# Kernel tuning notes

Hardware: AMD Instinct MI355X
Metric: run time of the kernel (lower is better)

Reference implementation:

```python
import jax, jax.numpy as jnp
import numpy as np

N, K, D = 500_000, 256, 64  # points, prototypes, feature dim


def setup_inputs() -> dict:
    key = jax.random.key(0)
    kx, km = jax.random.split(key)
    X = jax.random.normal(kx, (N, D), dtype=jnp.float32)
    mus = jax.random.normal(km, (K, D), dtype=jnp.float32)
    return {"X": X, "mus": mus}


def reference(X, mus):
    # Faithful to vmap(lambda x: argmin(sum((mus - x)**2, axis=1)))(X),
    # but expressed with the Gram-matrix distance trick so the K*D broadcast
    # is a single GEMM instead of an O(N,K,D) elementwise intermediate.
    x_sq = jnp.sum(X * X, axis=1, keepdims=True)        # [N, 1]
    mu_sq = jnp.sum(mus * mus, axis=1)                  # [K]
    d2 = x_sq - 2.0 * (X @ mus.T) + mu_sq[None, :]      # [N, K] squared dists
    return jnp.argmin(d2, axis=1)                       # [N] int assignments
```

## Files before the change

kernel.cpp:

```cpp
#include <hip/hip_runtime.h>


#define DIM 64
#define NPROTO 256
#define NBLK 1024
#define SUBT 4
#define PPI 64
#define MARGIN_ACC 0.005f

using f32x4  = __attribute__((ext_vector_type(4))) float;
using bf16x8 = __attribute__((ext_vector_type(8))) __bf16;
using bf16x4 = __attribute__((ext_vector_type(4))) __bf16;

__device__ __forceinline__ void split2(float x, __bf16& h0, __bf16& h1) {
    h0 = (__bf16)x;
    h1 = (__bf16)(x - (float)h0);
}

__device__ __forceinline__ void stage_one(__bf16* lvl0, float4 v, int wgi) {
    bf16x4 w0, w1;
    const float xf[4] = {v.x, v.y, v.z, v.w};
#pragma unroll
    for (int e = 0; e < 4; ++e) {
        __bf16 h0, h1;
        split2(xf[e], h0, h1);
        w0[e] = h0; w1[e] = h1;
    }
    ((bf16x4*)lvl0)[wgi] = w0;
    ((bf16x4*)(lvl0 + 16 * 64))[wgi] = w1;
}

__device__ __forceinline__ float4 loadx(const float* __restrict__ X, int t,
                                        int j, int srow, int spart, int n) {
    int pr = t * PPI + j * 16 + srow;
    pr = (pr < n) ? pr : (n - 1);
    return *(const float4*)(X + (size_t)pr * DIM + spart * 4);
}

__attribute__((amdgpu_waves_per_eu(3, 4)))
__global__ void __launch_bounds__(256)
argmin_mfma_kernel(const float* __restrict__ X,
                   const float* __restrict__ mus,
                   int* __restrict__ out,
                   unsigned* __restrict__ ws_count,
                   int* __restrict__ ws_list,
                   int use_list, int n) {
    __shared__ __align__(16) __bf16 s_x[2][SUBT][2][16][64];
    __shared__ float s_musq[NPROTO];
    __shared__ float s_cb[2][SUBT][4][16];
    __shared__ float s_cb2[2][SUBT][4][16];
    __shared__ int   s_ck[2][SUBT][4][16];

    const int tid = threadIdx.x;
    const int w  = tid >> 6;
    const int l  = tid & 63;
    const int lp = l & 15;
    const int lg = l >> 4;

    {
        const float4* m4 = (const float4*)(mus + tid * DIM);
        float a0 = 0.f, a1 = 0.f, a2 = 0.f, a3 = 0.f;
#pragma unroll
        for (int q = 0; q < 16; ++q) {
            float4 v = m4[q];
            a0 = fmaf(v.x, v.x, a0); a1 = fmaf(v.y, v.y, a1);
            a2 = fmaf(v.z, v.z, a2); a3 = fmaf(v.w, v.w, a3);
        }
        s_musq[tid] = -0.5f * ((a0 + a1) + (a2 + a3));
    }

    bf16x8 amu[4][2][2];
#pragma unroll
    for (int t = 0; t < 4; ++t) {
        const int p = w * 64 + t * 16 + lp;
#pragma unroll
        for (int h = 0; h < 2; ++h) {
            const float* src = mus + (size_t)p * DIM + h * 32 + lg * 8;
            const float4 va = *(const float4*)src;
            const float4 vb = *(const float4*)(src + 4);
            const float xs[8] = {va.x, va.y, va.z, va.w, vb.x, vb.y, vb.z, vb.w};
            bf16x8 m0, m1;
#pragma unroll
            for (int e = 0; e < 8; ++e) {
                __bf16 h0, h1;
                split2(xs[e], h0, h1);
                m0[e] = h0; m1[e] = h1;
            }
            amu[t][h][0] = m0; amu[t][h][1] = m1;
        }
    }

    const int ntiles = (n + PPI - 1) / PPI;
    const int q = ntiles / NBLK, rr = ntiles % NBLK;
    const int bid = blockIdx.x;
    const int t0  = bid * q + (bid < rr ? bid : rr);
    const int cnt = q + (bid < rr ? 1 : 0);

    const int srow = tid >> 4, spart = tid & 15;
    const int wgi = spart ^ ((srow & 7) << 1);

    float4 xn0 = loadx(X, t0, 0, srow, spart, n);
    float4 xn1 = loadx(X, t0, 1, srow, spart, n);
    float4 xn2 = loadx(X, t0, 2, srow, spart, n);
    float4 xn3 = loadx(X, t0, 3, srow, spart, n);
    stage_one(&s_x[0][0][0][srow][0], xn0, wgi);
    stage_one(&s_x[0][1][0][srow][0], xn1, wgi);
    stage_one(&s_x[0][2][0][srow][0], xn2, wgi);
    stage_one(&s_x[0][3][0][srow][0], xn3, wgi);
    __syncthreads();

    const int kbase = w * 64 + lg * 4;
    f32x4 mh[4];
#pragma unroll
    for (int t = 0; t < 4; ++t)
#pragma unroll
        for (int r = 0; r < 4; ++r)
            mh[t][r] = s_musq[kbase + t * 16 + r];

    for (int it = 0; it < cnt; ++it) {
        const int tile = t0 + it;
        const int par = it & 1;
        const bool more = (it + 1 < cnt);

        if (more) {
            xn0 = loadx(X, tile + 1, 0, srow, spart, n);
            xn1 = loadx(X, tile + 1, 1, srow, spart, n);
            xn2 = loadx(X, tile + 1, 2, srow, spart, n);
            xn3 = loadx(X, tile + 1, 3, srow, spart, n);
        }

#pragma unroll
        for (int j = 0; j < SUBT; ++j) {
            bf16x8 bx[2][2];
#pragma unroll
            for (int h = 0; h < 2; ++h)
#pragma unroll
                for (int v = 0; v < 2; ++v)
                    bx[h][v] = ((const bf16x8*)&s_x[par][j][v][lp][0])
                                   [(h * 4 + lg) ^ (lp & 7)];

            f32x4 acc[4];
#pragma unroll
            for (int t = 0; t < 4; ++t)
                acc[t] = __builtin_amdgcn_mfma_f32_16x16x32_bf16(
                    amu[t][0][0], bx[0][0], mh[t], 0, 0, 0);
#pragma unroll
            for (int t = 0; t < 4; ++t)
                acc[t] = __builtin_amdgcn_mfma_f32_16x16x32_bf16(
                    amu[t][1][0], bx[1][0], acc[t], 0, 0, 0);
            constexpr int PI[2] = {1, 0};
            constexpr int PJ[2] = {0, 1};
#pragma unroll
            for (int pp = 0; pp < 2; ++pp)
#pragma unroll
                for (int h = 0; h < 2; ++h)
#pragma unroll
                    for (int t = 0; t < 4; ++t)
                        acc[t] = __builtin_amdgcn_mfma_f32_16x16x32_bf16(
                            amu[t][h][PI[pp]], bx[h][PJ[pp]], acc[t], 0, 0, 0);

            float m1[8], m2[8];
            int   ka[8];
#pragma unroll
            for (int p = 0; p < 8; ++p) {
                const int t = p >> 1, rbase = (p & 1) * 2;
                const float da = acc[t][rbase], db = acc[t][rbase + 1];
                const bool gt = db > da;
                m1[p] = gt ? db : da;
                m2[p] = gt ? da : db;
                ka[p] = kbase + t * 16 + (gt ? rbase + 1 : rbase);
            }
#pragma unroll
            for (int lvl = 0; lvl < 3; ++lvl) {
                const int step = 1 << lvl;
#pragma unroll
                for (int p = 0; p < 8; p += 2 * step) {
                    const int pb = p + step;
                    const bool gt = m1[pb] > m1[p];
                    const float lo = fminf(m1[p], m1[pb]);
                    m1[p] = gt ? m1[pb] : m1[p];
                    ka[p] = gt ? ka[pb] : ka[p];
                    m2[p] = fmaxf(fmaxf(lo, m2[p]), m2[pb]);
                }
            }
            float b1 = m1[0], b2 = m2[0];
            int k1 = ka[0];

#pragma unroll
            for (int m = 16; m <= 32; m <<= 1) {
                const float ob1 = __shfl_xor(b1, m);
                const float ob2 = __shfl_xor(b2, m);
                const int   ok1 = __shfl_xor(k1, m);
                const float nb2 = fmaxf(fminf(b1, ob1), fmaxf(b2, ob2));
                const bool take = (ob1 > b1) || (ob1 == b1 && ok1 < k1);
                b1 = take ? ob1 : b1;
                k1 = take ? ok1 : k1;
                b2 = nb2;
            }
            if (lg == 0) {
                s_cb[par][j][w][lp] = b1;
                s_cb2[par][j][w][lp] = b2;
                s_ck[par][j][w][lp] = k1;
            }
        }

        if (more) {
            stage_one(&s_x[par ^ 1][0][0][srow][0], xn0, wgi);
            stage_one(&s_x[par ^ 1][1][0][srow][0], xn1, wgi);
            stage_one(&s_x[par ^ 1][2][0][srow][0], xn2, wgi);
            stage_one(&s_x[par ^ 1][3][0][srow][0], xn3, wgi);
        }

        __syncthreads();

        if (tid < PPI) {
            const int j = tid >> 4, c = tid & 15;
            float f1 = s_cb[par][j][0][c], f2 = s_cb2[par][j][0][c];
            int fk = s_ck[par][j][0][c];
#pragma unroll
            for (int ww = 1; ww < 4; ++ww) {
                const float ob1 = s_cb[par][j][ww][c];
                const float ob2 = s_cb2[par][j][ww][c];
                const int   ok1 = s_ck[par][j][ww][c];
                const float nb2 = fmaxf(fminf(f1, ob1), fmaxf(f2, ob2));
                if (ob1 > f1) { f1 = ob1; fk = ok1; }
                f2 = nb2;
            }
            const int i = tile * PPI + tid;
            if (i < n) {
                const bool close = (f1 - f2) < MARGIN_ACC;
                if (use_list) {
                    out[i] = fk;
                    if (close) {
                        const unsigned idx = atomicAdd(ws_count, 1u);
                        ws_list[idx] = i;
                    }
                } else {
                    out[i] = (int)((unsigned)fk | (close ? 0x80000000u : 0u));
                }
            }
        }
    }
}

__device__ __forceinline__ int recompute_point(const float* __restrict__ X,
                                               const float* __restrict__ mus,
                                               int pt, int l) {
    const float4* xr = (const float4*)(X + (size_t)pt * DIM);
    float4 xv[16];
    float xa0 = 0.f, xa1 = 0.f, xa2 = 0.f, xa3 = 0.f;
#pragma unroll
    for (int qq = 0; qq < 16; ++qq) {
        xv[qq] = xr[qq];
        xa0 = fmaf(xv[qq].x, xv[qq].x, xa0);
        xa1 = fmaf(xv[qq].y, xv[qq].y, xa1);
        xa2 = fmaf(xv[qq].z, xv[qq].z, xa2);
        xa3 = fmaf(xv[qq].w, xv[qq].w, xa3);
    }
    const float xsq = (xa0 + xa1) + (xa2 + xa3);
    float b1 = 3.4e38f; int k1 = 0;
#pragma unroll
    for (int e = 0; e < 4; ++e) {
        const int p = l * 4 + e;
        const float4* mr = (const float4*)(mus + (size_t)p * DIM);
        float d0 = 0.f, d1 = 0.f, d2a = 0.f, d3 = 0.f;
        float q0 = 0.f, q1 = 0.f, q2 = 0.f, q3 = 0.f;
#pragma unroll
        for (int qq = 0; qq < 16; ++qq) {
            const float4 mv = mr[qq];
            d0 = fmaf(mv.x, xv[qq].x, d0);
            d1 = fmaf(mv.y, xv[qq].y, d1);
            d2a = fmaf(mv.z, xv[qq].z, d2a);
            d3 = fmaf(mv.w, xv[qq].w, d3);
            q0 = fmaf(mv.x, mv.x, q0);
            q1 = fmaf(mv.y, mv.y, q1);
            q2 = fmaf(mv.z, mv.z, q2);
            q3 = fmaf(mv.w, mv.w, q3);
        }
        const float dot = (d0 + d1) + (d2a + d3);
        const float msq = (q0 + q1) + (q2 + q3);
        const float dd = (xsq - 2.0f * dot) + msq;
        if (dd < b1) { b1 = dd; k1 = p; }
    }
#pragma unroll
    for (int mm = 1; mm < 64; mm <<= 1) {
        const float ob = __shfl_xor(b1, mm);
        const int ok = __shfl_xor(k1, mm);
        if (ob < b1 || (ob == b1 && ok < k1)) { b1 = ob; k1 = ok; }
    }
    return k1;
}

__global__ void __launch_bounds__(256)
fixup_list_kernel(const float* __restrict__ X, const float* __restrict__ mus,
                  const unsigned* __restrict__ ws_count,
                  const int* __restrict__ ws_list, int* __restrict__ out) {
    const int gw = (int)((blockIdx.x * blockDim.x + threadIdx.x) >> 6);
    const int l  = threadIdx.x & 63;
    const int NW = (int)((gridDim.x * blockDim.x) >> 6);
    const int nf = (int)*ws_count;
    for (int j = gw; j < nf; j += NW) {
        const int pt = ws_list[j];
        const int k1 = recompute_point(X, mus, pt, l);
        if (l == 0) out[pt] = k1;
    }
}

__global__ void __launch_bounds__(256)
fixup_scan_kernel(const float* __restrict__ X, const float* __restrict__ mus,
                  int* __restrict__ out, int n) {
    const int gw = (int)((blockIdx.x * blockDim.x + threadIdx.x) >> 6);
    const int l  = threadIdx.x & 63;
    const int NW = (int)((gridDim.x * blockDim.x) >> 6);
    const int chunk = (n + NW - 1) / NW;
    const int base = gw * chunk;
    const int end  = (base + chunk < n) ? (base + chunk) : n;
    for (int s = base; s < end; s += 64) {
        const int i = s + l;
        const int v = (i < end) ? out[i] : 0;
        const bool fl = (i < end) && ((unsigned)v & 0x80000000u);
        unsigned long long m = __ballot(fl);
        while (m) {
            const int src = (int)__ffsll((unsigned long long)m) - 1;
            m &= m - 1;
            const int pt = __shfl(i, src);
            const int k1 = recompute_point(X, mus, pt, l);
            if (l == 0) out[pt] = k1;
        }
    }
}

extern "C" void kernel_launch(void* const* d_in, const int* in_sizes, int n_in,
                              void* d_out, int out_size, void* d_ws, size_t ws_size,
                              hipStream_t stream) {
    const float* X = (const float*)d_in[0];
    const float* mus = (const float*)d_in[1];
    int* out = (int*)d_out;
    const int n = in_sizes[0] / DIM;

    unsigned* ws_count = (unsigned*)d_ws;
    int* ws_list = (int*)((char*)d_ws + 16);
    const int use_list = (ws_size >= 16 + (size_t)n * 4) ? 1 : 0;

    if (use_list) {
        hipMemsetAsync(d_ws, 0, 16, stream);
    }

    argmin_mfma_kernel<<<NBLK, 256, 0, stream>>>(X, mus, out, ws_count,
                                                 ws_list, use_list, n);
    if (use_list) {
        fixup_list_kernel<<<512, 256, 0, stream>>>(X, mus, ws_count, ws_list,
                                                   out);
    } else {
        fixup_scan_kernel<<<512, 256, 0, stream>>>(X, mus, out, n);
    }
}
```

Measured before the change: 88.31 us.

## Switch distance GEMM from split-bf16 to single fp16 MFMA with wider margin

Replaces the two-term bf16 split of points and prototypes (four MFMA passes per tile) with a single fp16 conversion and one MFMA pass, halving the shared-memory staging and cutting the matrix work. To cover the lower precision, the near-tie margin that routes points to the exact fixup kernel is widened. It also raises the block count and occupancy hint, doubles the fixup grid, and simplifies the top-2 reduction with fmax/fmin. The risk is that more points fall inside the margin, which makes the fixup pass more expensive, and that an fp16 range or precision shortfall could misassign points whose gap exceeds the margin.

```diff
diff --git a/kernel.cpp b/kernel.cpp
--- a/kernel.cpp
+++ b/kernel.cpp
@@ -3,31 +3,18 @@
 
 #define DIM 64
 #define NPROTO 256
-#define NBLK 1024
+#define NBLK 1536
 #define SUBT 4
 #define PPI 64
-#define MARGIN_ACC 0.005f
-
-using f32x4  = __attribute__((ext_vector_type(4))) float;
-using bf16x8 = __attribute__((ext_vector_type(8))) __bf16;
-using bf16x4 = __attribute__((ext_vector_type(4))) __bf16;
-
-__device__ __forceinline__ void split2(float x, __bf16& h0, __bf16& h1) {
-    h0 = (__bf16)x;
-    h1 = (__bf16)(x - (float)h0);
-}
-
-__device__ __forceinline__ void stage_one(__bf16* lvl0, float4 v, int wgi) {
-    bf16x4 w0, w1;
-    const float xf[4] = {v.x, v.y, v.z, v.w};
-#pragma unroll
-    for (int e = 0; e < 4; ++e) {
-        __bf16 h0, h1;
-        split2(xf[e], h0, h1);
-        w0[e] = h0; w1[e] = h1;
-    }
-    ((bf16x4*)lvl0)[wgi] = w0;
-    ((bf16x4*)(lvl0 + 16 * 64))[wgi] = w1;
+#define MARGIN_ACC 0.015f
+
+using f32x4 = __attribute__((ext_vector_type(4))) float;
+using f16x8 = __attribute__((ext_vector_type(8))) _Float16;
+using f16x4 = __attribute__((ext_vector_type(4))) _Float16;
+
+__device__ __forceinline__ void stage_one(_Float16* row, float4 v, int wgi) {
+    f16x4 w0 = {(_Float16)v.x, (_Float16)v.y, (_Float16)v.z, (_Float16)v.w};
+    ((f16x4*)row)[wgi] = w0;
 }
 
 __device__ __forceinline__ float4 loadx(const float* __restrict__ X, int t,
@@ -37,7 +24,7 @@
     return *(const float4*)(X + (size_t)pr * DIM + spart * 4);
 }
 
-__attribute__((amdgpu_waves_per_eu(3, 4)))
+__attribute__((amdgpu_waves_per_eu(4, 8)))
 __global__ void __launch_bounds__(256)
 argmin_mfma_kernel(const float* __restrict__ X,
                    const float* __restrict__ mus,
@@ -45,7 +32,7 @@
                    unsigned* __restrict__ ws_count,
                    int* __restrict__ ws_list,
                    int use_list, int n) {
-    __shared__ __align__(16) __bf16 s_x[2][SUBT][2][16][64];
+    __shared__ __align__(16) _Float16 s_x[2][SUBT][16][64];
     __shared__ float s_musq[NPROTO];
     __shared__ float s_cb[2][SUBT][4][16];
     __shared__ float s_cb2[2][SUBT][4][16];
@@ -69,7 +56,7 @@
         s_musq[tid] = -0.5f * ((a0 + a1) + (a2 + a3));
     }
 
-    bf16x8 amu[4][2][2];
+    f16x8 amu[4][2];
 #pragma unroll
     for (int t = 0; t < 4; ++t) {
         const int p = w * 64 + t * 16 + lp;
@@ -78,15 +65,10 @@
             const float* src = mus + (size_t)p * DIM + h * 32 + lg * 8;
             const float4 va = *(const float4*)src;
             const float4 vb = *(const float4*)(src + 4);
-            const float xs[8] = {va.x, va.y, va.z, va.w, vb.x, vb.y, vb.z, vb.w};
-            bf16x8 m0, m1;
-#pragma unroll
-            for (int e = 0; e < 8; ++e) {
-                __bf16 h0, h1;
-                split2(xs[e], h0, h1);
-                m0[e] = h0; m1[e] = h1;
-            }
-            amu[t][h][0] = m0; amu[t][h][1] = m1;
+            f16x8 m0 = {(_Float16)va.x, (_Float16)va.y, (_Float16)va.z,
+                        (_Float16)va.w, (_Float16)vb.x, (_Float16)vb.y,
+                        (_Float16)vb.z, (_Float16)vb.w};
+            amu[t][h] = m0;
         }
     }
 
@@ -103,10 +85,10 @@
     float4 xn1 = loadx(X, t0, 1, srow, spart, n);
     float4 xn2 = loadx(X, t0, 2, srow, spart, n);
     float4 xn3 = loadx(X, t0, 3, srow, spart, n);
-    stage_one(&s_x[0][0][0][srow][0], xn0, wgi);
-    stage_one(&s_x[0][1][0][srow][0], xn1, wgi);
-    stage_one(&s_x[0][2][0][srow][0], xn2, wgi);
-    stage_one(&s_x[0][3][0][srow][0], xn3, wgi);
+    stage_one(&s_x[0][0][srow][0], xn0, wgi);
+    stage_one(&s_x[0][1][srow][0], xn1, wgi);
+    stage_one(&s_x[0][2][srow][0], xn2, wgi);
+    stage_one(&s_x[0][3][srow][0], xn3, wgi);
     __syncthreads();
 
     const int kbase = w * 64 + lg * 4;
@@ -131,33 +113,21 @@
 
 #pragma unroll
         for (int j = 0; j < SUBT; ++j) {
-            bf16x8 bx[2][2];
+            f16x8 bx[2];
 #pragma unroll
             for (int h = 0; h < 2; ++h)
-#pragma unroll
-                for (int v = 0; v < 2; ++v)
-                    bx[h][v] = ((const bf16x8*)&s_x[par][j][v][lp][0])
-                                   [(h * 4 + lg) ^ (lp & 7)];
+                bx[h] = ((const f16x8*)&s_x[par][j][lp][0])
+                            [(h * 4 + lg) ^ (lp & 7)];
 
             f32x4 acc[4];
 #pragma unroll
             for (int t = 0; t < 4; ++t)
-                acc[t] = __builtin_amdgcn_mfma_f32_16x16x32_bf16(
-                    amu[t][0][0], bx[0][0], mh[t], 0, 0, 0);
+                acc[t] = __builtin_amdgcn_mfma_f32_16x16x32_f16(
+                    amu[t][0], bx[0], mh[t], 0, 0, 0);
 #pragma unroll
             for (int t = 0; t < 4; ++t)
-                acc[t] = __builtin_amdgcn_mfma_f32_16x16x32_bf16(
-                    amu[t][1][0], bx[1][0], acc[t], 0, 0, 0);
-            constexpr int PI[2] = {1, 0};
-            constexpr int PJ[2] = {0, 1};
-#pragma unroll
-            for (int pp = 0; pp < 2; ++pp)
-#pragma unroll
-                for (int h = 0; h < 2; ++h)
-#pragma unroll
-                    for (int t = 0; t < 4; ++t)
-                        acc[t] = __builtin_amdgcn_mfma_f32_16x16x32_bf16(
-                            amu[t][h][PI[pp]], bx[h][PJ[pp]], acc[t], 0, 0, 0);
+                acc[t] = __builtin_amdgcn_mfma_f32_16x16x32_f16(
+                    amu[t][1], bx[1], acc[t], 0, 0, 0);
 
             float m1[8], m2[8];
             int   ka[8];
@@ -166,8 +136,8 @@
                 const int t = p >> 1, rbase = (p & 1) * 2;
                 const float da = acc[t][rbase], db = acc[t][rbase + 1];
                 const bool gt = db > da;
-                m1[p] = gt ? db : da;
-                m2[p] = gt ? da : db;
+                m1[p] = fmaxf(da, db);
+                m2[p] = fminf(da, db);
                 ka[p] = kbase + t * 16 + (gt ? rbase + 1 : rbase);
             }
 #pragma unroll
@@ -178,7 +148,7 @@
                     const int pb = p + step;
                     const bool gt = m1[pb] > m1[p];
                     const float lo = fminf(m1[p], m1[pb]);
-                    m1[p] = gt ? m1[pb] : m1[p];
+                    m1[p] = fmaxf(m1[p], m1[pb]);
                     ka[p] = gt ? ka[pb] : ka[p];
                     m2[p] = fmaxf(fmaxf(lo, m2[p]), m2[pb]);
                 }
@@ -191,11 +161,10 @@
                 const float ob1 = __shfl_xor(b1, m);
                 const float ob2 = __shfl_xor(b2, m);
                 const int   ok1 = __shfl_xor(k1, m);
-                const float nb2 = fmaxf(fminf(b1, ob1), fmaxf(b2, ob2));
-                const bool take = (ob1 > b1) || (ob1 == b1 && ok1 < k1);
-                b1 = take ? ob1 : b1;
+                const bool take = ob1 > b1;
+                b2 = fmaxf(fmaxf(fminf(b1, ob1), b2), ob2);
+                b1 = fmaxf(b1, ob1);
                 k1 = take ? ok1 : k1;
-                b2 = nb2;
             }
             if (lg == 0) {
                 s_cb[par][j][w][lp] = b1;
@@ -205,10 +174,10 @@
         }
 
         if (more) {
-            stage_one(&s_x[par ^ 1][0][0][srow][0], xn0, wgi);
-            stage_one(&s_x[par ^ 1][1][0][srow][0], xn1, wgi);
-            stage_one(&s_x[par ^ 1][2][0][srow][0], xn2, wgi);
-            stage_one(&s_x[par ^ 1][3][0][srow][0], xn3, wgi);
+            stage_one(&s_x[par ^ 1][0][srow][0], xn0, wgi);
+            stage_one(&s_x[par ^ 1][1][srow][0], xn1, wgi);
+            stage_one(&s_x[par ^ 1][2][srow][0], xn2, wgi);
+            stage_one(&s_x[par ^ 1][3][srow][0], xn3, wgi);
         }
 
         __syncthreads();
@@ -222,9 +191,10 @@
                 const float ob1 = s_cb[par][j][ww][c];
                 const float ob2 = s_cb2[par][j][ww][c];
                 const int   ok1 = s_ck[par][j][ww][c];
-                const float nb2 = fmaxf(fminf(f1, ob1), fmaxf(f2, ob2));
-                if (ob1 > f1) { f1 = ob1; fk = ok1; }
-                f2 = nb2;
+                const bool take = ob1 > f1;
+                f2 = fmaxf(fmaxf(fminf(f1, ob1), f2), ob2);
+                f1 = fmaxf(f1, ob1);
+                fk = take ? ok1 : fk;
             }
             const int i = tile * PPI + tid;
             if (i < n) {
@@ -349,8 +319,8 @@
     argmin_mfma_kernel<<<NBLK, 256, 0, stream>>>(X, mus, out, ws_count,
                                                  ws_list, use_list, n);
     if (use_list) {
-        fixup_list_kernel<<<512, 256, 0, stream>>>(X, mus, ws_count, ws_list,
-                                                   out);
+        fixup_list_kernel<<<1024, 256, 0, stream>>>(X, mus, ws_count, ws_list,
+                                                    out);
     } else {
         fixup_scan_kernel<<<512, 256, 0, stream>>>(X, mus, out, n);
     }
```

Result: slower. 105.0 us (+18.9%).
